# Optimization experiments

Hardware: AMD Instinct MI355X
Metric: run time of the kernel (lower is better)

Reference implementation:

```python
import jax, jax.numpy as jnp
import numpy as np
from jax import lax

START_IDX = 0
STOP_IDX = 1


def _forward_alg(feats_lbt, mask_lb, transitions):
    # feats_lbt: [L, B, T], mask_lb: [L, B], transitions[i, j] = score(j -> i)
    L, B, T = feats_lbt.shape
    init = jnp.full((B, T), -10000.0, dtype=feats_lbt.dtype).at[:, START_IDX].set(0.0)

    def step(fv, xs):
        feat, m = xs  # feat: [B, T], m: [B]
        # scores[b, next, prev] = fv[b, prev] + transitions[next, prev] + feat[b, next]
        scores = fv[:, None, :] + transitions[None, :, :] + feat[:, :, None]
        alphas = jax.nn.logsumexp(scores, axis=-1)  # [B, T]
        fv = jnp.where(m[:, None] > 0, alphas, fv)
        return fv, None

    fv, _ = lax.scan(step, init, (feats_lbt, mask_lb))
    terminal = fv + transitions[STOP_IDX][None, :]
    return jax.nn.logsumexp(terminal, axis=-1)  # [B]


def _score_sentence(feats_lbt, tags_bl, mask_lb, transitions):
    L, B, T = feats_lbt.shape
    start_col = jnp.full((B, 1), START_IDX, dtype=tags_bl.dtype)
    tags_ext = jnp.concatenate([start_col, tags_bl], axis=-1)  # [B, L+1]
    # transition scores along the gold path: [B, L]
    trans = transitions[tags_ext[:, 1:], tags_ext[:, :-1]]
    # emission scores: feats is [L, B, T] -> gather per-position gold tag
    emit = jnp.take_along_axis(
        feats_lbt, tags_bl.T[:, :, None], axis=-1
    )[:, :, 0]  # [L, B]
    step_scores = (trans.T + emit) * (mask_lb > 0)  # [L, B]
    score = step_scores.sum(axis=0)  # [B]
    lengths = mask_lb.sum(axis=0).astype(jnp.int32)  # [B]
    last_tag = tags_ext[jnp.arange(B), lengths]
    score = score + transitions[STOP_IDX, last_tag]
    return score


def setup_inputs() -> dict:
    key = jax.random.key(0)
    k1, k2, k3 = jax.random.split(key, 3)
    B, L, T = 256, 2048, 32
    efeats = jax.random.normal(k1, (B, L, T), dtype=jnp.float32)
    mask = jnp.ones((B, L), dtype=jnp.float32)
    tgt = jax.random.randint(k2, (B, L), 0, T, dtype=jnp.int32)
    transitions = jax.random.normal(k3, (T, T), dtype=jnp.float32)
    return {"efeats": efeats, "mask": mask, "tgt": tgt, "transitions": transitions}


def reference(efeats, mask, tgt, transitions):
    B, L = mask.shape
    mask_lb = mask.T  # [L, B]
    feats_lbt = jnp.transpose(efeats, (1, 0, 2))  # [L, B, T]
    forward_score = _forward_alg(feats_lbt, mask_lb, transitions)
    gold_score = _score_sentence(feats_lbt, tgt, mask_lb, transitions)
    loss = (forward_score - gold_score).sum() / B
    return loss
```

## Files before the change

### kernel.cpp

```cpp
#include <hip/hip_runtime.h>

#define B_SZ 256
#define L_SZ 2048
#define T_SZ 32
#define START_IDX 0
#define STOP_IDX 1

#define CLEN 128
#define NPAIR 64
#define NSLOT 8
#define NMAT_SEQ 2
#define NBLK_TOT (B_SZ * NMAT_SEQ)

#define FB_NCH 16
#define FB_CLEN 128

#define SCALE_LN 4.1588830833596718565f

typedef __attribute__((ext_vector_type(8))) short bf16x8;
typedef __attribute__((ext_vector_type(4))) float f32x4;
typedef __attribute__((ext_vector_type(2))) float f32x2;

__device__ __forceinline__ unsigned fau(float f){ union{float f; unsigned u;} v; v.f=f; return v.u; }
__device__ __forceinline__ float uaf(unsigned u){ union{unsigned u; float f;} v; v.u=u; return v.f; }
__device__ __forceinline__ int pack_trunc(float lo, float hi){
  return (int)__builtin_amdgcn_perm(fau(hi), fau(lo), 0x07060302u);
}
__device__ __forceinline__ bf16x8 frag_of(const int* p){
  union{ int i[4]; bf16x8 v; } u;
  u.i[0]=p[0]; u.i[1]=p[1]; u.i[2]=p[2]; u.i[3]=p[3];
  return u.v;
}

__device__ __forceinline__ void mfma4(bf16x8 A0, bf16x8 A1, bf16x8 B0, bf16x8 B1,
                                      f32x4& c00, f32x4& c01, f32x4& c10, f32x4& c11)
{
  const f32x4 z = {0.f,0.f,0.f,0.f};
  asm("s_nop 1\n\t"
      "v_mfma_f32_16x16x32_bf16 %0, %4, %5, %8\n\t"
      "v_mfma_f32_16x16x32_bf16 %1, %4, %6, %8\n\t"
      "v_mfma_f32_16x16x32_bf16 %2, %7, %5, %8\n\t"
      "v_mfma_f32_16x16x32_bf16 %3, %7, %6, %8\n\t"
      "s_nop 7\n\t"
      "s_nop 7"
      : "=&v"(c00), "=&v"(c01), "=&v"(c10), "=&v"(c11)
      : "v"(A0), "v"(B0), "v"(B1), "v"(A1), "v"(z));
}

__global__ void zero_kernel(float* out){ if(threadIdx.x==0) out[0]=0.f; }

__device__ __forceinline__ int mat_prod(const unsigned short* L, const unsigned short* Rt,
                                        unsigned short* dst, bool writeT, int lane)
{
  const int g = lane >> 4, c16 = lane & 15;
  const int ko = 8*g;
  bf16x8 A0 = *(const bf16x8*)(L  + (c16*T_SZ      + ko));
  bf16x8 A1 = *(const bf16x8*)(L  + ((16+c16)*T_SZ + ko));
  bf16x8 B0 = *(const bf16x8*)(Rt + (c16*T_SZ      + ko));
  bf16x8 B1 = *(const bf16x8*)(Rt + ((16+c16)*T_SZ + ko));
  f32x4 q00,q01,q10,q11;
  mfma4(A0, A1, B0, B1, q00, q01, q10, q11);

  unsigned mb = (unsigned)__builtin_amdgcn_readfirstlane((int)fau(q00[0]));
  int e = (int)((mb>>23)&255u) - 127;
  float r = uaf((unsigned)(127-e)<<23);
  #pragma unroll
  for (int i=0;i<4;++i){ q00[i]*=r; q01[i]*=r; q10[i]*=r; q11[i]*=r; }

  if (!writeT){
    #pragma unroll
    for (int reg=0; reg<4; ++reg){
      int x0 = 4*g + reg, x1 = 16 + 4*g + reg;
      dst[x0*T_SZ + c16]      = (unsigned short)(fau(q00[reg])>>16);
      dst[x0*T_SZ + 16 + c16] = (unsigned short)(fau(q01[reg])>>16);
      dst[x1*T_SZ + c16]      = (unsigned short)(fau(q10[reg])>>16);
      dst[x1*T_SZ + 16 + c16] = (unsigned short)(fau(q11[reg])>>16);
    }
  } else {
    #pragma unroll
    for (int rp=0; rp<2; ++rp){
      int xb0 = 4*g + 2*rp, xb1 = 16 + 4*g + 2*rp;
      *(int*)&dst[c16*T_SZ + xb0]        = pack_trunc(q00[2*rp], q00[2*rp+1]);
      *(int*)&dst[(16+c16)*T_SZ + xb0]   = pack_trunc(q01[2*rp], q01[2*rp+1]);
      *(int*)&dst[c16*T_SZ + xb1]        = pack_trunc(q10[2*rp], q10[2*rp+1]);
      *(int*)&dst[(16+c16)*T_SZ + xb1]   = pack_trunc(q11[2*rp], q11[2*rp+1]);
    }
  }
  return e;
}

__global__ __launch_bounds__(512, 4) void crf_chunk_kernel(
    const float* __restrict__ efeats, const float* __restrict__ mask,
    const int* __restrict__ tgt, const float* __restrict__ trans,
    unsigned short* __restrict__ wsM, int* __restrict__ wsE,
    float* __restrict__ wsG, float* __restrict__ wsL)
{
  __shared__ float s_trans[T_SZ*T_SZ];
  __shared__ float s_d[8][128];
  __shared__ unsigned short s_tree[NSLOT][T_SZ*T_SZ];
  __shared__ int   s_et[NSLOT];
  __shared__ float s_gd[8], s_ml[8];

  const int tid  = threadIdx.x;
  const int w    = tid >> 6;
  const int lane = tid & 63;
  const int g    = lane >> 4;
  const int c16  = lane & 15;

  const int b  = blockIdx.x >> 1;
  const int q  = blockIdx.x & 1;
  const int c  = q*NSLOT + w;
  const int l0 = c * CLEN;

  s_trans[tid]     = trans[tid];
  s_trans[tid+512] = trans[tid+512];
  __syncthreads();

  bf16x8 A0f, A1f;
  {
    int a0i[4], a1i[4];
    #pragma unroll
    for (int I=0; I<2; ++I){
      int row = 8*(c16>>2) + 4*I + (c16&3);
      float e[8];
      #pragma unroll
      for (int j=0;j<8;++j) e[j] = __expf(s_trans[row*T_SZ + 8*g + j]);
      int* dst = I ? a1i : a0i;
      #pragma unroll
      for (int p=0;p<4;++p) dst[p] = pack_trunc(e[2*p], e[2*p+1]);
    }
    A0f = frag_of(a0i); A1f = frag_of(a1i);
  }

  int b0[4], b1[4];
  #pragma unroll
  for (int p=0;p<4;++p){
    int s0 = 8*g + 2*p, s1 = s0+1;
    unsigned lo = (s0==c16)?0x3f80u:0u, hi = (s1==c16)?0x3f80u:0u;
    b0[p] = (int)(lo | (hi<<16));
    lo = (s0==16+c16)?0x3f80u:0u; hi = (s1==16+c16)?0x3f80u:0u;
    b1[p] = (int)(lo | (hi<<16));
  }

  const long fbase = ((long)b * L_SZ) * T_SZ;
  const int  mbase = b*L_SZ + l0;

  float mA = mask[mbase + lane];
  float mB = mask[mbase + 64 + lane];
  int   tA = tgt [mbase + lane];
  int   tB = tgt [mbase + 64 + lane];
  int   tpA = (l0 + lane == 0) ? START_IDX : tgt[mbase + lane - 1];
  int   tpB = tgt[mbase + 64 + lane - 1];

  float emA = efeats[fbase + (long)(l0+lane)*T_SZ + tA];
  float emB = efeats[fbase + (long)(l0+64+lane)*T_SZ + tB];
  float gl = ((mA > 0.f) ? (s_trans[tA*T_SZ + tpA] + emA) : 0.f)
           + ((mB > 0.f) ? (s_trans[tB*T_SZ + tpB] + emB) : 0.f);
  float ml = mA + mB;
  #pragma unroll
  for (int off=32; off>0; off>>=1){ gl += __shfl_xor(gl, off, 64); ml += __shfl_xor(ml, off, 64); }

  unsigned long long mb0 = __ballot(mA > 0.f);
  unsigned long long mb1 = __ballot(mB > 0.f);

  const float* fpt = efeats + fbase + (long)l0*T_SZ;
  float* s_dw = &s_d[w][0];

  float fq[4];
  #pragma unroll
  for (int i=1; i<=4; ++i) fq[i&3] = fpt[i*64 + lane];
  s_dw[lane] = __expf(fpt[lane] - SCALE_LN);

  if ((mb0 & mb1) == ~0ull){
    #pragma unroll 4
    for (int p=0; p<NPAIR; ++p){
      s_dw[((p+1)&1)*64 + lane] = __expf(fq[(p+1)&3] - SCALE_LN);
      int np = p+5; np = (np > NPAIR-1) ? (NPAIR-1) : np;
      fq[(p+1)&3] = fpt[np*64 + lane];
      const float* dbase = &s_dw[(p&1)*64];
      #pragma unroll
      for (int h=0; h<2; ++h){
        f32x4 c00,c01,c10,c11;
        mfma4(A0f, A1f, frag_of(b0), frag_of(b1), c00,c01,c10,c11);

        const float4* dv = (const float4*)(dbase + h*32);
        float4 dl = dv[2*g], dh2 = dv[2*g+1];
        f32x2 q0={c00[0],c00[1]}; q0 *= (f32x2){dl.x,dl.y};
        f32x2 q1={c00[2],c00[3]}; q1 *= (f32x2){dl.z,dl.w};
        f32x2 q2={c01[0],c01[1]}; q2 *= (f32x2){dl.x,dl.y};
        f32x2 q3={c01[2],c01[3]}; q3 *= (f32x2){dl.z,dl.w};
        f32x2 q4={c10[0],c10[1]}; q4 *= (f32x2){dh2.x,dh2.y};
        f32x2 q5={c10[2],c10[3]}; q5 *= (f32x2){dh2.z,dh2.w};
        f32x2 q6={c11[0],c11[1]}; q6 *= (f32x2){dh2.x,dh2.y};
        f32x2 q7={c11[2],c11[3]}; q7 *= (f32x2){dh2.z,dh2.w};

        b0[0]=pack_trunc(q0[0],q0[1]); b0[1]=pack_trunc(q1[0],q1[1]);
        b0[2]=pack_trunc(q4[0],q4[1]); b0[3]=pack_trunc(q5[0],q5[1]);
        b1[0]=pack_trunc(q2[0],q2[1]); b1[1]=pack_trunc(q3[0],q3[1]);
        b1[2]=pack_trunc(q6[0],q6[1]); b1[3]=pack_trunc(q7[0],q7[1]);
      }
    }
  } else {
    for (int p=0; p<NPAIR; ++p){
      s_dw[((p+1)&1)*64 + lane] = __expf(fq[(p+1)&3] - SCALE_LN);
      int np = p+5; if (np > NPAIR-1) np = NPAIR-1;
      fq[(p+1)&3] = fpt[np*64 + lane];
      const float* dbase = &s_dw[(p&1)*64];
      #pragma unroll
      for (int h=0; h<2; ++h){
        int t = 2*p + h;
        unsigned long long bit = (t < 64) ? (mb0 >> t) : (mb1 >> (t-64));
        if (bit & 1ull){
          f32x4 c00,c01,c10,c11;
          mfma4(A0f, A1f, frag_of(b0), frag_of(b1), c00,c01,c10,c11);

          const float4* dv = (const float4*)(dbase + h*32);
          float4 dl = dv[2*g], dh2 = dv[2*g+1];
          float f0=dl.x, f1=dl.y, f2=dl.z, f3=dl.w;
          float f4=dh2.x, f5=dh2.y, f6=dh2.z, f7=dh2.w;

          c00[0]*=f0; c00[1]*=f1; c00[2]*=f2; c00[3]*=f3;
          c01[0]*=f0; c01[1]*=f1; c01[2]*=f2; c01[3]*=f3;
          c10[0]*=f4; c10[1]*=f5; c10[2]*=f6; c10[3]*=f7;
          c11[0]*=f4; c11[1]*=f5; c11[2]*=f6; c11[3]*=f7;

          b0[0]=pack_trunc(c00[0],c00[1]); b0[1]=pack_trunc(c00[2],c00[3]);
          b0[2]=pack_trunc(c10[0],c10[1]); b0[3]=pack_trunc(c10[2],c10[3]);
          b1[0]=pack_trunc(c01[0],c01[1]); b1[1]=pack_trunc(c01[2],c01[3]);
          b1[2]=pack_trunc(c11[0],c11[1]); b1[3]=pack_trunc(c11[2],c11[3]);
        }
      }
    }
  }

  {
    unsigned short* S = &s_tree[w][0];
    if ((w & 1) == 0){
      #pragma unroll
      for (int p=0;p<4;++p){
        int s = 8*g + 2*p;
        *(int*)&S[c16*T_SZ + s]      = b0[p];
        *(int*)&S[(16+c16)*T_SZ + s] = b1[p];
      }
    } else {
      #pragma unroll
      for (int p=0;p<4;++p){
        int s = 8*g + 2*p;
        S[s*T_SZ + c16]          = (unsigned short)(b0[p] & 0xffff);
        S[(s+1)*T_SZ + c16]      = (unsigned short)(((unsigned)b0[p])>>16);
        S[s*T_SZ + 16 + c16]     = (unsigned short)(b1[p] & 0xffff);
        S[(s+1)*T_SZ + 16 + c16] = (unsigned short)(((unsigned)b1[p])>>16);
      }
    }
  }
  if (lane==0){
    s_et[w] = 6 * (__popcll(mb0) + __popcll(mb1));
    s_gd[w] = gl; s_ml[w] = ml;
  }
  __syncthreads();

  if (w < 4){
    int e = mat_prod(&s_tree[2*w][0], &s_tree[2*w+1][0], &s_tree[2*w][0], (w&1)!=0, lane);
    if (lane==0) s_et[2*w] = s_et[2*w] + s_et[2*w+1] + e;
  }
  __syncthreads();
  if (w < 2){
    int e = mat_prod(&s_tree[4*w][0], &s_tree[4*w+2][0], &s_tree[4*w][0], (w&1)!=0, lane);
    if (lane==0) s_et[4*w] = s_et[4*w] + s_et[4*w+2] + e;
  }
  __syncthreads();
  if (w == 0){
    int e = mat_prod(&s_tree[0][0], &s_tree[4][0], &s_tree[0][0], false, lane);
    if (lane==0) s_et[0] = s_et[0] + s_et[4] + e;
  }
  __syncthreads();

  const int bid = blockIdx.x;
  ((int*)(wsM + (long)bid*(T_SZ*T_SZ)))[tid] = ((const int*)&s_tree[0][0])[tid];
  if (tid == 0){
    wsE[bid] = s_et[0];
    float gs=0.f, ls=0.f;
    #pragma unroll
    for (int i=0;i<8;++i){ gs += s_gd[i]; ls += s_ml[i]; }
    wsG[bid] = gs; wsL[bid] = ls;
  }
}

__global__ __launch_bounds__(64) void crf_combine_kernel(
    const unsigned short* __restrict__ wsM, const int* __restrict__ wsE,
    const float* __restrict__ wsG, const float* __restrict__ wsL,
    const int* __restrict__ tgt, const float* __restrict__ trans,
    float* __restrict__ out)
{
  __shared__ unsigned short sM[NMAT_SEQ*T_SZ*T_SZ];
  __shared__ float s_v[T_SZ];

  const int tid = threadIdx.x;
  const int b   = blockIdx.x;

  const uint4* src = (const uint4*)(wsM + (long)b*NMAT_SEQ*T_SZ*T_SZ);
  #pragma unroll
  for (int i=0;i<4;++i) ((uint4*)sM)[tid + i*64] = src[tid + i*64];
  __syncthreads();

  const int s = tid & 31;
  float v = (s==START_IDX)?1.f:0.f;
  int E = 0;
  #pragma unroll
  for (int j=0; j<NMAT_SEQ; ++j){
    if (tid < 32) s_v[s] = v;
    __syncthreads();
    const unsigned short* M = &sM[j*T_SZ*T_SZ];
    float u = 0.f;
    #pragma unroll 8
    for (int x=0; x<T_SZ; ++x){
      float mv = uaf(((unsigned)M[x*T_SZ + s])<<16);
      u = fmaf(mv, s_v[x], u);
    }
    unsigned ub = (unsigned)__builtin_amdgcn_readfirstlane((int)fau(u));
    int eu = (int)((ub>>23)&255u)-127;
    E += wsE[b*NMAT_SEQ + j] + eu;
    v = u * uaf((unsigned)(127-eu)<<23);
    __syncthreads();
  }
  float term = v * __expf(trans[STOP_IDX*T_SZ + s]);
  #pragma unroll
  for (int off=16; off>0; off>>=1) term += __shfl_xor(term, off, 32);
  float fwd = (float)E * 0.69314718055994530942f + __logf(term);

  if (tid == 0){
    float gp = 0.f, lp = 0.f;
    #pragma unroll
    for (int j=0;j<NMAT_SEQ;++j){ gp += wsG[b*NMAT_SEQ+j]; lp += wsL[b*NMAT_SEQ+j]; }
    int len = (int)lp;
    int last_tag = (len==0)? START_IDX : tgt[b*L_SZ + len-1];
    float goldT = gp + trans[STOP_IDX*T_SZ + last_tag];
    atomicAdd(out, (fwd - goldT) * (1.0f/B_SZ));
  }
}

__global__ __launch_bounds__(1024) void crf_loss_kernel(
    const float* __restrict__ efeats, const float* __restrict__ mask,
    const int* __restrict__ tgt, const float* __restrict__ trans,
    float* __restrict__ out)
{
  __shared__ float s_trans[T_SZ*T_SZ];
  __shared__ float s_d[FB_NCH][T_SZ];
  __shared__ unsigned short s_M[FB_NCH][T_SZ*T_SZ];
  __shared__ int   s_es[FB_NCH];
  __shared__ float s_gd[FB_NCH];
  __shared__ float s_mlv[FB_NCH];

  const int tid  = threadIdx.x;
  const int b    = blockIdx.x;
  const int w    = tid >> 6;
  const int lane = tid & 63;
  const int g    = lane >> 4;
  const int c16  = lane & 15;
  const int i32  = lane & 31;

  s_trans[tid] = trans[tid];
  __syncthreads();

  int a0[4], a1[4];
  #pragma unroll
  for (int I=0; I<2; ++I){
    int row = 8*(c16>>2) + 4*I + (c16&3);
    float e[8];
    #pragma unroll
    for (int j=0;j<8;++j) e[j] = __expf(s_trans[row*T_SZ + 8*g + j]);
    int* dst = I ? a1 : a0;
    #pragma unroll
    for (int p=0;p<4;++p) dst[p] = pack_trunc(e[2*p], e[2*p+1]);
  }

  int b0[4], b1[4];
  #pragma unroll
  for (int p=0;p<4;++p){
    int s0 = 8*g + 2*p, s1 = s0+1;
    unsigned lo = (s0==c16)?0x3f80u:0u, hi = (s1==c16)?0x3f80u:0u;
    b0[p] = (int)(lo | (hi<<16));
    lo = (s0==16+c16)?0x3f80u:0u; hi = (s1==16+c16)?0x3f80u:0u;
    b1[p] = (int)(lo | (hi<<16));
  }

  const int l0 = w * FB_CLEN;
  const long fbase = ((long)b * L_SZ) * T_SZ;

  float fqv[4];
  #pragma unroll
  for (int i=0;i<4;++i) fqv[i] = efeats[fbase + (long)(l0+i)*T_SZ + i32];

  int   tA = tgt [b*L_SZ + l0 + lane];
  int   tB = tgt [b*L_SZ + l0 + 64 + lane];
  float mA = mask[b*L_SZ + l0 + lane];
  float mB = mask[b*L_SZ + l0 + 64 + lane];
  int prev = (l0==0) ? START_IDX : tgt[b*L_SZ + l0 - 1];

  int esum = 0;
  float gold = 0.f, mlen = 0.f;
  const f32x4 zf = {0.f,0.f,0.f,0.f};

  #pragma unroll 4
  for (int t=0; t<FB_CLEN; ++t){
    float fcur = fqv[t&3];
    int lpf = l0 + t + 4; lpf = (lpf < L_SZ) ? lpf : (L_SZ-1);
    fqv[t&3] = efeats[fbase + (long)lpf*T_SZ + i32];

    float mk  = uaf((unsigned)__builtin_amdgcn_readlane((int)fau((t<64)?mA:mB), t&63));
    int   cur = __builtin_amdgcn_readlane((t<64)?tA:tB, t&63);
    mlen += mk;

    if (mk > 0.f){
      if (lane < 32) s_d[w][lane] = __expf(fcur);

      f32x4 c00 = __builtin_amdgcn_mfma_f32_16x16x32_bf16(frag_of(a0), frag_of(b0), zf, 0,0,0);
      f32x4 c01 = __builtin_amdgcn_mfma_f32_16x16x32_bf16(frag_of(a0), frag_of(b1), zf, 0,0,0);
      f32x4 c10 = __builtin_amdgcn_mfma_f32_16x16x32_bf16(frag_of(a1), frag_of(b0), zf, 0,0,0);
      f32x4 c11 = __builtin_amdgcn_mfma_f32_16x16x32_bf16(frag_of(a1), frag_of(b1), zf, 0,0,0);

      const float4* dv = (const float4*)(&s_d[w][0]);
      float4 dl = dv[2*g], dh = dv[2*g+1];
      float f0=dl.x, f1=dl.y, f2=dl.z, f3=dl.w;
      float f4=dh.x, f5=dh.y, f6=dh.z, f7=dh.w;

      float m00 = c00[0]*f0;
      unsigned mb = (unsigned)__builtin_amdgcn_readfirstlane((int)fau(m00));
      int e = (int)((mb>>23)&255u) - 127;
      esum += e;
      float r = uaf((unsigned)(127-e)<<23);
      f0*=r; f1*=r; f2*=r; f3*=r; f4*=r; f5*=r; f6*=r; f7*=r;

      c00[0]*=f0; c00[1]*=f1; c00[2]*=f2; c00[3]*=f3;
      c01[0]*=f0; c01[1]*=f1; c01[2]*=f2; c01[3]*=f3;
      c10[0]*=f4; c10[1]*=f5; c10[2]*=f6; c10[3]*=f7;
      c11[0]*=f4; c11[1]*=f5; c11[2]*=f6; c11[3]*=f7;

      b0[0]=pack_trunc(c00[0],c00[1]); b0[1]=pack_trunc(c00[2],c00[3]);
      b0[2]=pack_trunc(c10[0],c10[1]); b0[3]=pack_trunc(c10[2],c10[3]);
      b1[0]=pack_trunc(c01[0],c01[1]); b1[1]=pack_trunc(c01[2],c01[3]);
      b1[2]=pack_trunc(c11[0],c11[1]); b1[3]=pack_trunc(c11[2],c11[3]);

      float tp   = s_trans[cur*T_SZ + prev];
      float emit = uaf((unsigned)__builtin_amdgcn_readlane((int)fau(fcur), cur));
      gold += tp + emit;
    }
    prev = cur;
  }

  #pragma unroll
  for (int p=0;p<4;++p){
    int s = 8*g + 2*p;
    *(int*)((char*)(&s_M[w][0]) + (((long)(c16   )*T_SZ + s) * 2)) = b0[p];
    *(int*)((char*)(&s_M[w][0]) + (((long)(16+c16)*T_SZ + s) * 2)) = b1[p];
  }
  if (lane==0){ s_es[w]=esum; s_gd[w]=gold; s_mlv[w]=mlen; }
  __syncthreads();

  if (w==0){
    int s = i32;
    float v = (s==START_IDX)?1.f:0.f;
    int E = 0;
    for (int c=0;c<FB_NCH;++c){
      float u=0.f;
      #pragma unroll 8
      for (int k=0;k<T_SZ;++k){
        float mv = uaf(((unsigned)s_M[c][k*T_SZ + s])<<16);
        float vk = uaf((unsigned)__builtin_amdgcn_readlane((int)fau(v), k));
        u = fmaf(mv, vk, u);
      }
      unsigned ub = (unsigned)__builtin_amdgcn_readfirstlane((int)fau(u));
      int eu = (int)((ub>>23)&255u)-127;
      E += s_es[c] + eu;
      v = u * uaf((unsigned)(127-eu)<<23);
    }
    float term = v * __expf(s_trans[STOP_IDX*T_SZ + s]);
    #pragma unroll
    for (int off=16; off>0; off>>=1) term += __shfl_xor(term, off, 32);
    float fwd = (float)E * 0.69314718055994530942f + __logf(term);

    float gp = (s<FB_NCH)? s_gd[s] : 0.f;
    float lp = (s<FB_NCH)? s_mlv[s] : 0.f;
    #pragma unroll
    for (int off=16; off>0; off>>=1){ gp += __shfl_xor(gp, off, 32); lp += __shfl_xor(lp, off, 32); }
    int len = (int)lp;
    int last_tag = (len==0)? START_IDX : tgt[b*L_SZ + (len-1)];
    float goldT = gp + s_trans[STOP_IDX*T_SZ + last_tag];
    if (tid==0) atomicAdd(out, (fwd - goldT) * (1.0f/B_SZ));
  }
}

extern "C" void kernel_launch(void* const* d_in, const int* in_sizes, int n_in,
                              void* d_out, int out_size, void* d_ws, size_t ws_size,
                              hipStream_t stream)
{
  const float* efeats = (const float*)d_in[0];
  const float* mask   = (const float*)d_in[1];
  const int*   tgt    = (const int*)d_in[2];
  const float* trans  = (const float*)d_in[3];
  float* out = (float*)d_out;

  const size_t needM = (size_t)NBLK_TOT * T_SZ * T_SZ * 2;
  const size_t need  = needM + (size_t)NBLK_TOT * 12;

  zero_kernel<<<dim3(1), dim3(64), 0, stream>>>(out);

  if (ws_size >= need){
    unsigned short* wsM = (unsigned short*)d_ws;
    char* p = (char*)d_ws + needM;
    int*   wsE = (int*)p;
    float* wsG = (float*)(p + (size_t)NBLK_TOT*4);
    float* wsL = (float*)(p + (size_t)NBLK_TOT*8);
    crf_chunk_kernel<<<dim3(NBLK_TOT), dim3(512), 0, stream>>>(
        efeats, mask, tgt, trans, wsM, wsE, wsG, wsL);
    crf_combine_kernel<<<dim3(B_SZ), dim3(64), 0, stream>>>(
        wsM, wsE, wsG, wsL, tgt, trans, out);
  } else {
    crf_loss_kernel<<<dim3(B_SZ), dim3(1024), 0, stream>>>(efeats, mask, tgt, trans, out);
  }
}
```

Measured before the change: 141.3 us.

## Pair adjacent steps into a leaf matrix product off the serial MFMA chain

In the fully-unmasked path, each pair of timesteps is now merged into one 32x32 matrix product, (diag(d)·E)·(E·diag(d')). It is computed independently of the running state one iteration ahead, so the dependent chain does one MFMA group per pair instead of two. The elementwise scaling moves off the critical path into the leaf computation, which can overlap with the serial multiply. In exchange it adds independent MFMA work and more registers for the transposed exp(trans) tables, and it rounds to bf16 at different points.

```diff
diff --git a/kernel.cpp b/kernel.cpp
--- a/kernel.cpp
+++ b/kernel.cpp
@@ -89,6 +89,31 @@
   return e;
 }
 
+__device__ __forceinline__ void leaf_product(const float* dbuf, int sig0, int g,
+    const float* EA0, const float* EA1, const float* EB0, const float* EB1,
+    int* An0, int* An1)
+{
+  const float4* dv = (const float4*)dbuf;
+  float4 da0 = dv[2*g], da1 = dv[2*g+1];
+  float d_b0 = dbuf[32 + sig0];
+  float d_b1 = dbuf[32 + sig0 + 4];
+  float dA[8] = {da0.x,da0.y,da0.z,da0.w,da1.x,da1.y,da1.z,da1.w};
+  int AL0[4], AL1[4], BL0[4], BL1[4];
+  #pragma unroll
+  for (int t=0;t<4;++t){
+    AL0[t] = pack_trunc(EA0[2*t]*dA[2*t], EA0[2*t+1]*dA[2*t+1]);
+    AL1[t] = pack_trunc(EA1[2*t]*dA[2*t], EA1[2*t+1]*dA[2*t+1]);
+    BL0[t] = pack_trunc(EB0[2*t]*d_b0,    EB0[2*t+1]*d_b0);
+    BL1[t] = pack_trunc(EB1[2*t]*d_b1,    EB1[2*t+1]*d_b1);
+  }
+  f32x4 p00,p01,p10,p11;
+  mfma4(frag_of(AL0), frag_of(AL1), frag_of(BL0), frag_of(BL1), p00,p01,p10,p11);
+  An0[0]=pack_trunc(p00[0],p00[1]); An0[1]=pack_trunc(p00[2],p00[3]);
+  An0[2]=pack_trunc(p10[0],p10[1]); An0[3]=pack_trunc(p10[2],p10[3]);
+  An1[0]=pack_trunc(p01[0],p01[1]); An1[1]=pack_trunc(p01[2],p01[3]);
+  An1[2]=pack_trunc(p11[0],p11[1]); An1[3]=pack_trunc(p11[2],p11[3]);
+}
+
 __global__ __launch_bounds__(512, 4) void crf_chunk_kernel(
     const float* __restrict__ efeats, const float* __restrict__ mask,
     const int* __restrict__ tgt, const float* __restrict__ trans,
@@ -115,32 +140,6 @@
   s_trans[tid]     = trans[tid];
   s_trans[tid+512] = trans[tid+512];
   __syncthreads();
-
-  bf16x8 A0f, A1f;
-  {
-    int a0i[4], a1i[4];
-    #pragma unroll
-    for (int I=0; I<2; ++I){
-      int row = 8*(c16>>2) + 4*I + (c16&3);
-      float e[8];
-      #pragma unroll
-      for (int j=0;j<8;++j) e[j] = __expf(s_trans[row*T_SZ + 8*g + j]);
-      int* dst = I ? a1i : a0i;
-      #pragma unroll
-      for (int p=0;p<4;++p) dst[p] = pack_trunc(e[2*p], e[2*p+1]);
-    }
-    A0f = frag_of(a0i); A1f = frag_of(a1i);
-  }
-
-  int b0[4], b1[4];
-  #pragma unroll
-  for (int p=0;p<4;++p){
-    int s0 = 8*g + 2*p, s1 = s0+1;
-    unsigned lo = (s0==c16)?0x3f80u:0u, hi = (s1==c16)?0x3f80u:0u;
-    b0[p] = (int)(lo | (hi<<16));
-    lo = (s0==16+c16)?0x3f80u:0u; hi = (s1==16+c16)?0x3f80u:0u;
-    b1[p] = (int)(lo | (hi<<16));
-  }
 
   const long fbase = ((long)b * L_SZ) * T_SZ;
   const int  mbase = b*L_SZ + l0;
@@ -166,41 +165,82 @@
   const float* fpt = efeats + fbase + (long)l0*T_SZ;
   float* s_dw = &s_d[w][0];
 
-  float fq[4];
-  #pragma unroll
-  for (int i=1; i<=4; ++i) fq[i&3] = fpt[i*64 + lane];
-  s_dw[lane] = __expf(fpt[lane] - SCALE_LN);
+  const int sig0 = 8*(c16>>2) + (c16&3);
+
+  int Bm0[4], Bm1[4];
+  #pragma unroll
+  for (int p=0;p<4;++p){
+    int s0 = 8*g + 2*p, s1 = s0+1;
+    unsigned lo = (s0==c16)?0x3f80u:0u, hi = (s1==c16)?0x3f80u:0u;
+    Bm0[p] = (int)(lo | (hi<<16));
+    lo = (s0==16+c16)?0x3f80u:0u; hi = (s1==16+c16)?0x3f80u:0u;
+    Bm1[p] = (int)(lo | (hi<<16));
+  }
 
   if ((mb0 & mb1) == ~0ull){
-    #pragma unroll 4
+    float EA0[8], EA1[8], EB0[8], EB1[8];
+    #pragma unroll
+    for (int j=0;j<8;++j){
+      int row = 8*g + j;
+      EA0[j] = __expf(s_trans[row*T_SZ + sig0    ]);
+      EA1[j] = __expf(s_trans[row*T_SZ + sig0 + 4]);
+      EB0[j] = __expf(s_trans[(sig0    )*T_SZ + row]);
+      EB1[j] = __expf(s_trans[(sig0 + 4)*T_SZ + row]);
+    }
+
+    float f0 = fpt[lane];
+    float f1 = fpt[64 + lane];
+    s_dw[lane]      = __expf(f0 - SCALE_LN);
+    s_dw[64 + lane] = __expf(f1 - SCALE_LN);
+    float fq[4];
+    fq[2] = fpt[2*64+lane]; fq[3] = fpt[3*64+lane];
+    fq[0] = fpt[4*64+lane]; fq[1] = fpt[5*64+lane];
+
+    int Ac0[4], Ac1[4], An0[4], An1[4];
+    leaf_product(&s_dw[0], sig0, g, EA0, EA1, EB0, EB1, Ac0, Ac1);
+
+    #pragma unroll 2
     for (int p=0; p<NPAIR; ++p){
-      s_dw[((p+1)&1)*64 + lane] = __expf(fq[(p+1)&3] - SCALE_LN);
-      int np = p+5; np = (np > NPAIR-1) ? (NPAIR-1) : np;
-      fq[(p+1)&3] = fpt[np*64 + lane];
-      const float* dbase = &s_dw[(p&1)*64];
+      if (p < NPAIR-2){
+        s_dw[(p&1)*64 + lane] = __expf(fq[(p+2)&3] - SCALE_LN);
+        int np = p+6; np = (np > NPAIR-1) ? (NPAIR-1) : np;
+        fq[(p+2)&3] = fpt[np*64 + lane];
+      }
+      if (p < NPAIR-1)
+        leaf_product(&s_dw[((p+1)&1)*64], sig0, g, EA0, EA1, EB0, EB1, An0, An1);
+
+      f32x4 cc00,cc01,cc10,cc11;
+      mfma4(frag_of(Ac0), frag_of(Ac1), frag_of(Bm0), frag_of(Bm1), cc00,cc01,cc10,cc11);
+      Bm0[0]=pack_trunc(cc00[0],cc00[1]); Bm0[1]=pack_trunc(cc00[2],cc00[3]);
+      Bm0[2]=pack_trunc(cc10[0],cc10[1]); Bm0[3]=pack_trunc(cc10[2],cc10[3]);
+      Bm1[0]=pack_trunc(cc01[0],cc01[1]); Bm1[1]=pack_trunc(cc01[2],cc01[3]);
+      Bm1[2]=pack_trunc(cc11[0],cc11[1]); Bm1[3]=pack_trunc(cc11[2],cc11[3]);
+
       #pragma unroll
-      for (int h=0; h<2; ++h){
-        f32x4 c00,c01,c10,c11;
-        mfma4(A0f, A1f, frag_of(b0), frag_of(b1), c00,c01,c10,c11);
-
-        const float4* dv = (const float4*)(dbase + h*32);
-        float4 dl = dv[2*g], dh2 = dv[2*g+1];
-        f32x2 q0={c00[0],c00[1]}; q0 *= (f32x2){dl.x,dl.y};
-        f32x2 q1={c00[2],c00[3]}; q1 *= (f32x2){dl.z,dl.w};
-        f32x2 q2={c01[0],c01[1]}; q2 *= (f32x2){dl.x,dl.y};
-        f32x2 q3={c01[2],c01[3]}; q3 *= (f32x2){dl.z,dl.w};
-        f32x2 q4={c10[0],c10[1]}; q4 *= (f32x2){dh2.x,dh2.y};
-        f32x2 q5={c10[2],c10[3]}; q5 *= (f32x2){dh2.z,dh2.w};
-        f32x2 q6={c11[0],c11[1]}; q6 *= (f32x2){dh2.x,dh2.y};
-        f32x2 q7={c11[2],c11[3]}; q7 *= (f32x2){dh2.z,dh2.w};
-
-        b0[0]=pack_trunc(q0[0],q0[1]); b0[1]=pack_trunc(q1[0],q1[1]);
-        b0[2]=pack_trunc(q4[0],q4[1]); b0[3]=pack_trunc(q5[0],q5[1]);
-        b1[0]=pack_trunc(q2[0],q2[1]); b1[1]=pack_trunc(q3[0],q3[1]);
-        b1[2]=pack_trunc(q6[0],q6[1]); b1[3]=pack_trunc(q7[0],q7[1]);
+      for (int t=0;t<4;++t){ Ac0[t]=An0[t]; Ac1[t]=An1[t]; }
+    }
+  } else {
+    bf16x8 A0f, A1f;
+    {
+      int a0i[4], a1i[4];
+      #pragma unroll
+      for (int I=0; I<2; ++I){
+        int row = 8*(c16>>2) + 4*I + (c16&3);
+        float e[8];
+        #pragma unroll
+        for (int j=0;j<8;++j) e[j] = __expf(s_trans[row*T_SZ + 8*g + j]);
+        int* dst = I ? a1i : a0i;
+        #pragma unroll
+        for (int p=0;p<4;++p) dst[p] = pack_trunc(e[2*p], e[2*p+1]);
       }
-    }
-  } else {
+      A0f = frag_of(a0i); A1f = frag_of(a1i);
+    }
+
+    float fq[4];
+    #pragma unroll
+    for (int i=1; i<=4; ++i) fq[i&3] = fpt[i*64 + lane];
+    s_dw[lane] = __expf(fpt[lane] - SCALE_LN);
+
     for (int p=0; p<NPAIR; ++p){
       s_dw[((p+1)&1)*64 + lane] = __expf(fq[(p+1)&3] - SCALE_LN);
       int np = p+5; if (np > NPAIR-1) np = NPAIR-1;
@@ -212,7 +252,7 @@
         unsigned long long bit = (t < 64) ? (mb0 >> t) : (mb1 >> (t-64));
         if (bit & 1ull){
           f32x4 c00,c01,c10,c11;
-          mfma4(A0f, A1f, frag_of(b0), frag_of(b1), c00,c01,c10,c11);
+          mfma4(A0f, A1f, frag_of(Bm0), frag_of(Bm1), c00,c01,c10,c11);
 
           const float4* dv = (const float4*)(dbase + h*32);
           float4 dl = dv[2*g], dh2 = dv[2*g+1];
@@ -224,10 +264,10 @@
           c10[0]*=f4; c10[1]*=f5; c10[2]*=f6; c10[3]*=f7;
           c11[0]*=f4; c11[1]*=f5; c11[2]*=f6; c11[3]*=f7;
 
-          b0[0]=pack_trunc(c00[0],c00[1]); b0[1]=pack_trunc(c00[2],c00[3]);
-          b0[2]=pack_trunc(c10[0],c10[1]); b0[3]=pack_trunc(c10[2],c10[3]);
-          b1[0]=pack_trunc(c01[0],c01[1]); b1[1]=pack_trunc(c01[2],c01[3]);
-          b1[2]=pack_trunc(c11[0],c11[1]); b1[3]=pack_trunc(c11[2],c11[3]);
+          Bm0[0]=pack_trunc(c00[0],c00[1]); Bm0[1]=pack_trunc(c00[2],c00[3]);
+          Bm0[2]=pack_trunc(c10[0],c10[1]); Bm0[3]=pack_trunc(c10[2],c10[3]);
+          Bm1[0]=pack_trunc(c01[0],c01[1]); Bm1[1]=pack_trunc(c01[2],c01[3]);
+          Bm1[2]=pack_trunc(c11[0],c11[1]); Bm1[3]=pack_trunc(c11[2],c11[3]);
         }
       }
     }
@@ -239,17 +279,17 @@
       #pragma unroll
       for (int p=0;p<4;++p){
         int s = 8*g + 2*p;
-        *(int*)&S[c16*T_SZ + s]      = b0[p];
-        *(int*)&S[(16+c16)*T_SZ + s] = b1[p];
+        *(int*)&S[c16*T_SZ + s]      = Bm0[p];
+        *(int*)&S[(16+c16)*T_SZ + s] = Bm1[p];
       }
     } else {
       #pragma unroll
       for (int p=0;p<4;++p){
         int s = 8*g + 2*p;
-        S[s*T_SZ + c16]          = (unsigned short)(b0[p] & 0xffff);
-        S[(s+1)*T_SZ + c16]      = (unsigned short)(((unsigned)b0[p])>>16);
-        S[s*T_SZ + 16 + c16]     = (unsigned short)(b1[p] & 0xffff);
-        S[(s+1)*T_SZ + 16 + c16] = (unsigned short)(((unsigned)b1[p])>>16);
+        S[s*T_SZ + c16]          = (unsigned short)(Bm0[p] & 0xffff);
+        S[(s+1)*T_SZ + c16]      = (unsigned short)(((unsigned)Bm0[p])>>16);
+        S[s*T_SZ + 16 + c16]     = (unsigned short)(Bm1[p] & 0xffff);
+        S[(s+1)*T_SZ + 16 + c16] = (unsigned short)(((unsigned)Bm1[p])>>16);
       }
     }
   }
```

After: 151.0 us. +6.8%, slower.

## Fold emission scaling into per-step A matrix instead of scaling MFMA outputs

Applied to the files above, without the earlier changes.

In the all-unmasked fast path, each step now builds the A operand as exp(trans) times the per-row emission factor, computed in registers, and feeds it to the MFMA. The running matrix is then just repacked, so the post-MFMA multiply by emission values read from shared memory goes away. Each lane also loads its own emission rows straight from global memory with an 8-deep register prefetch ring, replacing the LDS double-buffer staging. The cost is one pack-and-multiply of A per step and strided per-lane global loads.

```diff
diff --git a/kernel.cpp b/kernel.cpp
--- a/kernel.cpp
+++ b/kernel.cpp
@@ -116,32 +116,6 @@
   s_trans[tid+512] = trans[tid+512];
   __syncthreads();
 
-  bf16x8 A0f, A1f;
-  {
-    int a0i[4], a1i[4];
-    #pragma unroll
-    for (int I=0; I<2; ++I){
-      int row = 8*(c16>>2) + 4*I + (c16&3);
-      float e[8];
-      #pragma unroll
-      for (int j=0;j<8;++j) e[j] = __expf(s_trans[row*T_SZ + 8*g + j]);
-      int* dst = I ? a1i : a0i;
-      #pragma unroll
-      for (int p=0;p<4;++p) dst[p] = pack_trunc(e[2*p], e[2*p+1]);
-    }
-    A0f = frag_of(a0i); A1f = frag_of(a1i);
-  }
-
-  int b0[4], b1[4];
-  #pragma unroll
-  for (int p=0;p<4;++p){
-    int s0 = 8*g + 2*p, s1 = s0+1;
-    unsigned lo = (s0==c16)?0x3f80u:0u, hi = (s1==c16)?0x3f80u:0u;
-    b0[p] = (int)(lo | (hi<<16));
-    lo = (s0==16+c16)?0x3f80u:0u; hi = (s1==16+c16)?0x3f80u:0u;
-    b1[p] = (int)(lo | (hi<<16));
-  }
-
   const long fbase = ((long)b * L_SZ) * T_SZ;
   const int  mbase = b*L_SZ + l0;
 
@@ -164,43 +138,81 @@
   unsigned long long mb1 = __ballot(mB > 0.f);
 
   const float* fpt = efeats + fbase + (long)l0*T_SZ;
-  float* s_dw = &s_d[w][0];
-
-  float fq[4];
-  #pragma unroll
-  for (int i=1; i<=4; ++i) fq[i&3] = fpt[i*64 + lane];
-  s_dw[lane] = __expf(fpt[lane] - SCALE_LN);
+  const int sig0 = 8*(c16>>2) + (c16&3);
+
+  int Bm0[4], Bm1[4];
+  #pragma unroll
+  for (int p=0;p<4;++p){
+    int s0 = 8*g + 2*p, s1 = s0+1;
+    unsigned lo = (s0==c16)?0x3f80u:0u, hi = (s1==c16)?0x3f80u:0u;
+    Bm0[p] = (int)(lo | (hi<<16));
+    lo = (s0==16+c16)?0x3f80u:0u; hi = (s1==16+c16)?0x3f80u:0u;
+    Bm1[p] = (int)(lo | (hi<<16));
+  }
 
   if ((mb0 & mb1) == ~0ull){
-    #pragma unroll 4
-    for (int p=0; p<NPAIR; ++p){
-      s_dw[((p+1)&1)*64 + lane] = __expf(fq[(p+1)&3] - SCALE_LN);
-      int np = p+5; np = (np > NPAIR-1) ? (NPAIR-1) : np;
-      fq[(p+1)&3] = fpt[np*64 + lane];
-      const float* dbase = &s_dw[(p&1)*64];
+    f32x2 EA0[4], EA1[4];
+    #pragma unroll
+    for (int p=0;p<4;++p){
+      EA0[p] = (f32x2){ __expf(s_trans[(sig0  )*T_SZ + 8*g + 2*p]),
+                        __expf(s_trans[(sig0  )*T_SZ + 8*g + 2*p+1]) };
+      EA1[p] = (f32x2){ __expf(s_trans[(sig0+4)*T_SZ + 8*g + 2*p]),
+                        __expf(s_trans[(sig0+4)*T_SZ + 8*g + 2*p+1]) };
+    }
+
+    const float* fL = fpt + sig0;
+    const float* fH = fpt + sig0 + 4;
+    float f0r[8], f1r[8];
+    #pragma unroll
+    for (int i=0;i<8;++i){ f0r[i] = fL[i*T_SZ]; f1r[i] = fH[i*T_SZ]; }
+
+    #pragma unroll 8
+    for (int t=0; t<CLEN; ++t){
+      const int r = t & 7;
+      float d0 = __expf(f0r[r] - SCALE_LN);
+      float d1 = __expf(f1r[r] - SCALE_LN);
+      int nt = t + 8; nt = (nt > CLEN-1) ? (CLEN-1) : nt;
+      f0r[r] = fL[nt*T_SZ]; f1r[r] = fH[nt*T_SZ];
+
+      f32x2 dd0 = {d0, d0}, dd1 = {d1, d1};
+      int A0[4], A1[4];
       #pragma unroll
-      for (int h=0; h<2; ++h){
-        f32x4 c00,c01,c10,c11;
-        mfma4(A0f, A1f, frag_of(b0), frag_of(b1), c00,c01,c10,c11);
-
-        const float4* dv = (const float4*)(dbase + h*32);
-        float4 dl = dv[2*g], dh2 = dv[2*g+1];
-        f32x2 q0={c00[0],c00[1]}; q0 *= (f32x2){dl.x,dl.y};
-        f32x2 q1={c00[2],c00[3]}; q1 *= (f32x2){dl.z,dl.w};
-        f32x2 q2={c01[0],c01[1]}; q2 *= (f32x2){dl.x,dl.y};
-        f32x2 q3={c01[2],c01[3]}; q3 *= (f32x2){dl.z,dl.w};
-        f32x2 q4={c10[0],c10[1]}; q4 *= (f32x2){dh2.x,dh2.y};
-        f32x2 q5={c10[2],c10[3]}; q5 *= (f32x2){dh2.z,dh2.w};
-        f32x2 q6={c11[0],c11[1]}; q6 *= (f32x2){dh2.x,dh2.y};
-        f32x2 q7={c11[2],c11[3]}; q7 *= (f32x2){dh2.z,dh2.w};
-
-        b0[0]=pack_trunc(q0[0],q0[1]); b0[1]=pack_trunc(q1[0],q1[1]);
-        b0[2]=pack_trunc(q4[0],q4[1]); b0[3]=pack_trunc(q5[0],q5[1]);
-        b1[0]=pack_trunc(q2[0],q2[1]); b1[1]=pack_trunc(q3[0],q3[1]);
-        b1[2]=pack_trunc(q6[0],q6[1]); b1[3]=pack_trunc(q7[0],q7[1]);
+      for (int p=0;p<4;++p){
+        f32x2 u = EA0[p] * dd0;  A0[p] = pack_trunc(u[0], u[1]);
+        f32x2 v = EA1[p] * dd1;  A1[p] = pack_trunc(v[0], v[1]);
       }
+
+      f32x4 c00,c01,c10,c11;
+      mfma4(frag_of(A0), frag_of(A1), frag_of(Bm0), frag_of(Bm1), c00,c01,c10,c11);
+
+      Bm0[0]=pack_trunc(c00[0],c00[1]); Bm0[1]=pack_trunc(c00[2],c00[3]);
+      Bm0[2]=pack_trunc(c10[0],c10[1]); Bm0[3]=pack_trunc(c10[2],c10[3]);
+      Bm1[0]=pack_trunc(c01[0],c01[1]); Bm1[1]=pack_trunc(c01[2],c01[3]);
+      Bm1[2]=pack_trunc(c11[0],c11[1]); Bm1[3]=pack_trunc(c11[2],c11[3]);
     }
   } else {
+    bf16x8 A0f, A1f;
+    {
+      int a0i[4], a1i[4];
+      #pragma unroll
+      for (int I=0; I<2; ++I){
+        int row = 8*(c16>>2) + 4*I + (c16&3);
+        float e[8];
+        #pragma unroll
+        for (int j=0;j<8;++j) e[j] = __expf(s_trans[row*T_SZ + 8*g + j]);
+        int* dst = I ? a1i : a0i;
+        #pragma unroll
+        for (int p=0;p<4;++p) dst[p] = pack_trunc(e[2*p], e[2*p+1]);
+      }
+      A0f = frag_of(a0i); A1f = frag_of(a1i);
+    }
+
+    float* s_dw = &s_d[w][0];
+    float fq[4];
+    #pragma unroll
+    for (int i=1; i<=4; ++i) fq[i&3] = fpt[i*64 + lane];
+    s_dw[lane] = __expf(fpt[lane] - SCALE_LN);
+
     for (int p=0; p<NPAIR; ++p){
       s_dw[((p+1)&1)*64 + lane] = __expf(fq[(p+1)&3] - SCALE_LN);
       int np = p+5; if (np > NPAIR-1) np = NPAIR-1;
@@ -212,7 +224,7 @@
         unsigned long long bit = (t < 64) ? (mb0 >> t) : (mb1 >> (t-64));
         if (bit & 1ull){
           f32x4 c00,c01,c10,c11;
-          mfma4(A0f, A1f, frag_of(b0), frag_of(b1), c00,c01,c10,c11);
+          mfma4(A0f, A1f, frag_of(Bm0), frag_of(Bm1), c00,c01,c10,c11);
 
           const float4* dv = (const float4*)(dbase + h*32);
           float4 dl = dv[2*g], dh2 = dv[2*g+1];
@@ -224,10 +236,10 @@
           c10[0]*=f4; c10[1]*=f5; c10[2]*=f6; c10[3]*=f7;
           c11[0]*=f4; c11[1]*=f5; c11[2]*=f6; c11[3]*=f7;
 
-          b0[0]=pack_trunc(c00[0],c00[1]); b0[1]=pack_trunc(c00[2],c00[3]);
-          b0[2]=pack_trunc(c10[0],c10[1]); b0[3]=pack_trunc(c10[2],c10[3]);
-          b1[0]=pack_trunc(c01[0],c01[1]); b1[1]=pack_trunc(c01[2],c01[3]);
-          b1[2]=pack_trunc(c11[0],c11[1]); b1[3]=pack_trunc(c11[2],c11[3]);
+          Bm0[0]=pack_trunc(c00[0],c00[1]); Bm0[1]=pack_trunc(c00[2],c00[3]);
+          Bm0[2]=pack_trunc(c10[0],c10[1]); Bm0[3]=pack_trunc(c10[2],c10[3]);
+          Bm1[0]=pack_trunc(c01[0],c01[1]); Bm1[1]=pack_trunc(c01[2],c01[3]);
+          Bm1[2]=pack_trunc(c11[0],c11[1]); Bm1[3]=pack_trunc(c11[2],c11[3]);
         }
       }
     }
@@ -239,17 +251,17 @@
       #pragma unroll
       for (int p=0;p<4;++p){
         int s = 8*g + 2*p;
-        *(int*)&S[c16*T_SZ + s]      = b0[p];
-        *(int*)&S[(16+c16)*T_SZ + s] = b1[p];
+        *(int*)&S[c16*T_SZ + s]      = Bm0[p];
+        *(int*)&S[(16+c16)*T_SZ + s] = Bm1[p];
       }
     } else {
       #pragma unroll
       for (int p=0;p<4;++p){
         int s = 8*g + 2*p;
-        S[s*T_SZ + c16]          = (unsigned short)(b0[p] & 0xffff);
-        S[(s+1)*T_SZ + c16]      = (unsigned short)(((unsigned)b0[p])>>16);
-        S[s*T_SZ + 16 + c16]     = (unsigned short)(b1[p] & 0xffff);
-        S[(s+1)*T_SZ + 16 + c16] = (unsigned short)(((unsigned)b1[p])>>16);
+        S[s*T_SZ + c16]          = (unsigned short)(Bm0[p] & 0xffff);
+        S[(s+1)*T_SZ + c16]      = (unsigned short)(((unsigned)Bm0[p])>>16);
+        S[s*T_SZ + 16 + c16]     = (unsigned short)(Bm1[p] & 0xffff);
+        S[(s+1)*T_SZ + 16 + c16] = (unsigned short)(((unsigned)Bm1[p])>>16);
       }
     }
   }
```

Result: slower. 149.3 us (+5.6%).
